# Optimization experiments

Measured on AMD Instinct MI355X. Metric: run time of the kernel, lower is better.

## Reference

```python
import math
import jax, jax.numpy as jnp
import numpy as np

B, S, E, H = 4, 2048, 1024, 16
D = E // H


def setup_inputs() -> dict:
    key = jax.random.key(0)
    k1, k2, k3 = jax.random.split(key, 3)
    return {
        "hidden_state": jax.random.normal(k1, (B, S, E), dtype=jnp.float32),
        "attention_mask": jnp.zeros((B, 1, 1, S), dtype=jnp.float32),
        "W_attn": jax.random.normal(k2, (E, 3 * E), dtype=jnp.float32) * 0.02,
        "b_attn": jnp.zeros((3 * E,), dtype=jnp.float32),
        "W_proj": jax.random.normal(k3, (E, E), dtype=jnp.float32) * 0.02,
        "b_proj": jnp.zeros((E,), dtype=jnp.float32),
    }


def reference(hidden_state, attention_mask, W_attn, b_attn, W_proj, b_proj):
    b, s, e = hidden_state.shape
    d = e // H
    # c_attn (HF Conv1D): x @ W + b -> [B,S,3E]
    x = hidden_state @ W_attn + b_attn
    q, k, v = jnp.split(x, 3, axis=-1)
    # split heads -> [B,H,S,D]
    q = q.reshape(b, s, H, d).transpose(0, 2, 1, 3)
    k = k.reshape(b, s, H, d).transpose(0, 2, 1, 3)
    v = v.reshape(b, s, H, d).transpose(0, 2, 1, 3)
    # scores [B,H,S,S]; scale=True divides by sqrt(d_head)
    w = jnp.einsum("bhqd,bhkd->bhqk", q, k) / math.sqrt(d)
    causal = jnp.tril(jnp.ones((s, s), dtype=w.dtype))[None, None]
    w = w * causal + (-10000.0) * (1.0 - causal)
    w = w + attention_mask
    w = jax.nn.softmax(w, axis=-1)  # attn_dropout p=0 (eval)
    out = jnp.einsum("bhqk,bhkd->bhqd", w, v)
    # merge heads -> [B,S,E]
    out = out.transpose(0, 2, 1, 3).reshape(b, s, e)
    # c_proj; resid_dropout p=0 (eval)
    return out @ W_proj + b_proj
```

## Files before the change

### kernel.cpp

```cpp
#include <hip/hip_runtime.h>
#include <hip/hip_bf16.h>

typedef __attribute__((ext_vector_type(4))) float f32x4;
typedef __attribute__((ext_vector_type(8))) short bf16x8;

#define B_SZ  4
#define S_LEN 2048
#define EMB   1024
#define NH    16
#define DH    64
#define E3    3072
#define QKLD  2048
#define LOG2E 1.4426950408889634f
#define SC2   (0.125f * LOG2E)
#define MSTAT 14.0f

__device__ __forceinline__ void gload_lds16(const void* g, void* l) {
  __builtin_amdgcn_global_load_lds((const __attribute__((address_space(1))) void*)g,
                                   (__attribute__((address_space(3))) void*)l, 16, 0, 0);
}

__global__ void cvt_bf16_kernel(const float* __restrict__ in,
                                __hip_bfloat16* __restrict__ out, int n) {
  const int i = (blockIdx.x * 256 + threadIdx.x) * 4;
  if (i >= n) return;
  const float4 v = *(const float4*)(in + i);
  __align__(8) __hip_bfloat16 o[4];
  o[0] = __float2bfloat16(v.x); o[1] = __float2bfloat16(v.y);
  o[2] = __float2bfloat16(v.z); o[3] = __float2bfloat16(v.w);
  *(uint2*)(out + i) = *(const uint2*)o;
}

__global__ __launch_bounds__(256)
void transpose_cvt(const float* __restrict__ in, __hip_bfloat16* __restrict__ out,
                   int R, int C) {
  __shared__ float tile[32][33];
  const int tx = threadIdx.x & 31, ty = threadIdx.x >> 5;
  const int c = blockIdx.x * 32 + tx;
#pragma unroll
  for (int i = 0; i < 32; i += 8)
    tile[ty + i][tx] = in[(size_t)(blockIdx.y * 32 + ty + i) * C + c];
  __syncthreads();
  const int r2 = blockIdx.y * 32 + tx;
#pragma unroll
  for (int i = 0; i < 32; i += 8)
    out[(size_t)(blockIdx.x * 32 + ty + i) * R + r2] = __float2bfloat16(tile[tx][ty + i]);
}

__global__ __launch_bounds__(256)
void gemm_bt_f32(const __hip_bfloat16* __restrict__ A, const __hip_bfloat16* __restrict__ BT,
                 const float* __restrict__ bias, float* __restrict__ Cout,
                 int M, int N, int K, int ldc) {
  __shared__ __align__(16) __hip_bfloat16 As[128 * 32];
  __shared__ __align__(16) __hip_bfloat16 Bs[128 * 32];
  const int tid = threadIdx.x;
  const int lane = tid & 63, w = tid >> 6;
  const int lr = lane & 15, lg = lane >> 4;
  const int wr = w >> 1, wc = w & 1;
  const int m0 = blockIdx.x * 128, n0 = blockIdx.y * 128;

  f32x4 acc[4][4] = {};

  for (int k0 = 0; k0 < K; k0 += 32) {
    __syncthreads();
#pragma unroll
    for (int rr = 0; rr < 2; ++rr) {
      const int base = rr * 4096 + w * 1024;
      const int idx = base + lane * 16;
      const int row = idx >> 6;
      const int col = (idx & 63) >> 1;
      gload_lds16(A + (size_t)(m0 + row) * K + k0 + col, (char*)As + base);
      gload_lds16(BT + (size_t)(n0 + row) * K + k0 + col, (char*)Bs + base);
    }
    __syncthreads();
    bf16x8 af[4], bg[4];
#pragma unroll
    for (int m = 0; m < 4; ++m)
      af[m] = *(const bf16x8*)&As[(wr * 64 + m * 16 + lr) * 32 + lg * 8];
#pragma unroll
    for (int n = 0; n < 4; ++n)
      bg[n] = *(const bf16x8*)&Bs[(wc * 64 + n * 16 + lr) * 32 + lg * 8];
#pragma unroll
    for (int m = 0; m < 4; ++m)
#pragma unroll
      for (int n = 0; n < 4; ++n)
        acc[m][n] = __builtin_amdgcn_mfma_f32_16x16x32_bf16(af[m], bg[n], acc[m][n], 0, 0, 0);
  }

#pragma unroll
  for (int m = 0; m < 4; ++m)
#pragma unroll
    for (int n = 0; n < 4; ++n) {
      const int col = n0 + wc * 64 + n * 16 + lr;
      const float bv = bias[col];
#pragma unroll
      for (int r = 0; r < 4; ++r) {
        const int rowg = m0 + wr * 64 + m * 16 + lg * 4 + r;
        Cout[(size_t)rowg * ldc + col] = acc[m][n][r] + bv;
      }
    }
}


#define SBAR() { __builtin_amdgcn_s_barrier(); __builtin_amdgcn_sched_barrier(0); }
#define VMCNT(N) asm volatile("s_waitcnt vmcnt(" #N ")" ::: "memory")

#define STG_A(T, H, BUF) { \
    const __hip_bfloat16* s_ = pA + (size_t)((H) * 128) * 1024 + (T) * 64; \
    gload_lds16(s_, (BUF) + (H) * 16384 + w * 1024 + lane * 16); \
    gload_lds16(s_ + 65536, (BUF) + (H) * 16384 + 8192 + w * 1024 + lane * 16); }

#define STG_B(T, H, BUF) { \
    const __hip_bfloat16* s_ = pB + (size_t)((H) * 128) * 1024 + (T) * 64; \
    gload_lds16(s_, (BUF) + (H) * 16384 + w * 1024 + lane * 16); \
    gload_lds16(s_ + 65536, (BUF) + (H) * 16384 + 8192 + w * 1024 + lane * 16); }

#define RD_A(BUF, MH) { _Pragma("unroll") for (int m_ = 0; m_ < 4; ++m_) { \
    a[m_][0] = *(const bf16x8*)((BUF) + arow + ((MH) * 64 + m_ * 16) * 128 + sw0); \
    a[m_][1] = *(const bf16x8*)((BUF) + arow + ((MH) * 64 + m_ * 16) * 128 + sw1); } }

#define RD_B(BUF, NH, BARR) { _Pragma("unroll") for (int n_ = 0; n_ < 2; ++n_) { \
    BARR[n_][0] = *(const bf16x8*)((BUF) + brow + ((NH) * 32 + n_ * 16) * 128 + sw0); \
    BARR[n_][1] = *(const bf16x8*)((BUF) + brow + ((NH) * 32 + n_ * 16) * 128 + sw1); } }

#define MQUAD(MH, NH, BARR) { __builtin_amdgcn_s_setprio(1); \
    _Pragma("unroll") for (int m_ = 0; m_ < 4; ++m_) \
    _Pragma("unroll") for (int n_ = 0; n_ < 2; ++n_) \
    _Pragma("unroll") for (int k_ = 0; k_ < 2; ++k_) \
      acc[(MH)*4+m_][(NH)*2+n_] = __builtin_amdgcn_mfma_f32_16x16x32_bf16( \
          a[m_][k_], BARR[n_][k_], acc[(MH)*4+m_][(NH)*2+n_], 0, 0, 0); \
    __builtin_amdgcn_s_setprio(0); }

__global__ __launch_bounds__(512, 2)
void gemm_qkv_8ph(const __hip_bfloat16* __restrict__ A, const __hip_bfloat16* __restrict__ BT,
                  const float* __restrict__ bias, __hip_bfloat16* __restrict__ qkOut,
                  __hip_bfloat16* __restrict__ vt) {
  __shared__ __attribute__((aligned(16))) char lds[131072];
  char* const As0 = lds;
  char* const As1 = lds + 32768;
  char* const Bs0 = lds + 65536;
  char* const Bs1 = lds + 98304;

  const int tid = threadIdx.x;
  const int lane = tid & 63, w = tid >> 6;
  const int lr = lane & 15, lg = lane >> 4, lg4 = lg * 4;
  const int wm = w >> 2, wn = w & 3;
  const int m0 = blockIdx.x * 256, n0 = blockIdx.y * 256;

  const int srl = lane >> 3;
  const int scol = ((lane & 7) ^ srl) * 8;
  const __hip_bfloat16* pA = A + (size_t)(m0 + w * 8 + srl) * 1024 + scol;
  const __hip_bfloat16* pB = BT + (size_t)(n0 + w * 8 + srl) * 1024 + scol;

  const int sw0 = (lg ^ (lr & 7)) << 4;
  const int sw1 = sw0 ^ 0x40;
  const int arow = (wm * 128 + lr) * 128;
  const int brow = (wn * 64 + lr) * 128;

  f32x4 acc[8][4] = {};
  bf16x8 a[4][2], b0[2][2], b1[2][2];

  STG_A(0, 0, As0); STG_B(0, 0, Bs0); STG_A(0, 1, As0); STG_B(0, 1, Bs0); STG_A(1, 0, As1);
  VMCNT(2);
  SBAR();

  auto iter = [&](int t0, bool more) {
    RD_A(As0, 0); RD_B(Bs0, 0, b0);
    STG_B(t0 + 1, 0, Bs1);
    SBAR(); MQUAD(0, 0, b0); SBAR();
    RD_B(Bs0, 1, b1);
    STG_A(t0 + 1, 1, As1);
    SBAR(); MQUAD(0, 1, b1); SBAR();
    RD_A(As0, 1); RD_B(Bs0, 0, b0);
    STG_B(t0 + 1, 1, Bs1);
    SBAR(); MQUAD(1, 0, b0); SBAR();
    RD_B(Bs0, 1, b1);
    if (more) { STG_A(t0 + 2, 0, As0); VMCNT(2); } else { VMCNT(0); }
    SBAR(); MQUAD(1, 1, b1); SBAR();
    RD_A(As1, 0); RD_B(Bs1, 0, b0);
    if (more) STG_B(t0 + 2, 0, Bs0);
    SBAR(); MQUAD(0, 0, b0); SBAR();
    RD_B(Bs1, 1, b1);
    if (more) STG_A(t0 + 2, 1, As0);
    SBAR(); MQUAD(0, 1, b1); SBAR();
    RD_A(As1, 1); RD_B(Bs1, 0, b0);
    if (more) STG_B(t0 + 2, 1, Bs0);
    SBAR(); MQUAD(1, 0, b0); SBAR();
    RD_B(Bs1, 1, b1);
    if (more) { STG_A(t0 + 3, 0, As1); VMCNT(2); }
    SBAR(); MQUAD(1, 1, b1); SBAR();
  };

#pragma unroll 1
  for (int i = 0; i < 7; ++i) iter(2 * i, true);
  iter(14, false);

  if (n0 >= 2 * EMB) {
#pragma unroll
    for (int m8 = 0; m8 < 8; ++m8) {
      const int rowg0 = m0 + wm * 128 + m8 * 16 + lg4;
      const int bz = rowg0 >> 11, sloc = rowg0 & (S_LEN - 1);
#pragma unroll
      for (int n4 = 0; n4 < 4; ++n4) {
        const int col = n0 + wn * 64 + n4 * 16 + lr;
        const int c2 = col - 2 * EMB;
        const int hh = c2 >> 6, dd = c2 & 63;
        const float bv = bias[col];
        __align__(8) __hip_bfloat16 pb[4];
#pragma unroll
        for (int r = 0; r < 4; ++r) pb[r] = __float2bfloat16(acc[m8][n4][r] + bv);
        *(uint2*)&vt[(size_t)((bz * NH + hh) * DH + dd) * S_LEN + sloc] = *(const uint2*)pb;
      }
    }
  } else {
#pragma unroll
    for (int m8 = 0; m8 < 8; ++m8) {
#pragma unroll
      for (int n4 = 0; n4 < 4; ++n4) {
        const int col = n0 + wn * 64 + n4 * 16 + lr;
        const float bv = bias[col];
#pragma unroll
        for (int r = 0; r < 4; ++r) {
          const int rowg = m0 + wm * 128 + m8 * 16 + lg4 + r;
          qkOut[(size_t)rowg * QKLD + col] = __float2bfloat16(acc[m8][n4][r] + bv);
        }
      }
    }
  }
}

template <bool DIAG>
__device__ __forceinline__ void qstep(const char* Ks, const char* Vs,
                                      __hip_bfloat16 (*Psw)[72], const float* Ms,
                                      int msoff, const bf16x8 (&aq)[2], f32x4 (&acc)[4],
                                      float& lrun, int lr, int lg, int lg4, int wq) {
  f32x4 sacc[4] = {};
  __builtin_amdgcn_s_setprio(1);
#pragma unroll
  for (int kt = 0; kt < 4; ++kt)
#pragma unroll
    for (int ks = 0; ks < 2; ++ks) {
      const bf16x8 kb = *(const bf16x8*)(Ks + (kt * 16 + lr) * 128 +
                                         (((ks * 4 + lg) ^ (lr & 7)) << 4));
      sacc[kt] = __builtin_amdgcn_mfma_f32_16x16x32_bf16(kb, aq[ks], sacc[kt], 0, 0, 0);
    }
  __builtin_amdgcn_s_setprio(0);
#pragma unroll
  for (int kt = 0; kt < 4; ++kt) {
    const f32x4 mk = *(const f32x4*)&Ms[msoff + kt * 16 + lg4];
    float pp[4];
    __align__(8) __hip_bfloat16 pb[4];
#pragma unroll
    for (int r = 0; r < 4; ++r) {
      float sv = sacc[kt][r] * SC2 + mk[r];
      if (DIAG && (kt * 16 + lg4 + r > wq)) sv = -1.0e9f;
      pp[r] = exp2f(sv);
      pb[r] = __float2bfloat16(pp[r]);
    }
    lrun += (pp[0] + pp[1]) + (pp[2] + pp[3]);
    *(uint2*)&Psw[lr][kt * 16 + lg4] = *(const uint2*)pb;
  }
#pragma unroll
  for (int ks = 0; ks < 2; ++ks) {
    const bf16x8 pa = *(const bf16x8*)&Psw[lr][ks * 32 + lg * 8];
    __builtin_amdgcn_s_setprio(1);
#pragma unroll
    for (int dt = 0; dt < 4; ++dt) {
      const bf16x8 vb = *(const bf16x8*)(Vs + (dt * 16 + lr) * 128 +
                                         (((ks * 4 + lg) ^ (lr & 7)) << 4));
      acc[dt] = __builtin_amdgcn_mfma_f32_16x16x32_bf16(pa, vb, acc[dt], 0, 0, 0);
    }
    __builtin_amdgcn_s_setprio(0);
  }
}

#define STAGE_LOAD_BUMP()                                                          \
  {                                                                                \
    kpre[0] = *(const bf16x8*)kcur;                                                \
    kpre[1] = *(const bf16x8*)(kcur + 8 * QKLD);                                   \
    vpre[0] = *(const bf16x8*)vcur;                                                \
    vpre[1] = *(const bf16x8*)(vcur + 8 * S_LEN);                                  \
    kcur += 64 * QKLD;                                                             \
    vcur += 64;                                                                    \
  }

#define TILE_SYNC(PREFETCH)                                                        \
  {                                                                                \
    __syncthreads();                                                               \
    *(bf16x8*)kw0 = kpre[0];                                                       \
    *(bf16x8*)(kw0 + 1024) = kpre[1];                                              \
    *(bf16x8*)vw0 = vpre[0];                                                       \
    *(bf16x8*)(vw0 + 1024) = vpre[1];                                              \
    __syncthreads();                                                               \
    if (PREFETCH) STAGE_LOAD_BUMP();                                               \
  }

__global__ __launch_bounds__(256, 4)
void flash_attn5(const __hip_bfloat16* __restrict__ qk, const __hip_bfloat16* __restrict__ vt,
                 const float* __restrict__ amask, __hip_bfloat16* __restrict__ aout) {
  const int x = blockIdx.x;
  const int h = blockIdx.y, bz = blockIdx.z;
  const int tid = threadIdx.x;
  const int lane = tid & 63, w = tid >> 6;
  const int lr = lane & 15, lg = lane >> 4, lg4 = lg * 4;
  const int wq = w * 16 + lr;

  const int qta = x, qtb = 31 - x;

  __shared__ __align__(16) __hip_bfloat16 Ks[64 * 64];
  __shared__ __align__(16) __hip_bfloat16 Vs[64 * 64];
  __shared__ __align__(16) __hip_bfloat16 Ps[4][16][72];
  __shared__ __align__(16) float Ms[S_LEN];

#pragma unroll
  for (int i = 0; i < 2; ++i) {
    const int e = (i * 256 + tid) * 4;
    const f32x4 mv = *(const f32x4*)&amask[bz * S_LEN + e];
    f32x4 r;
#pragma unroll
    for (int j = 0; j < 4; ++j) r[j] = mv[j] * LOG2E - MSTAT;
    *(f32x4*)&Ms[e] = r;
  }

  bf16x8 aqA[2], aqB[2];
  {
    const __hip_bfloat16* qpA =
        qk + (size_t)(bz * S_LEN + qta * 64 + w * 16 + lr) * QKLD + h * DH + lg * 8;
    aqA[0] = *(const bf16x8*)qpA; aqA[1] = *(const bf16x8*)(qpA + 32);
    const __hip_bfloat16* qpB =
        qk + (size_t)(bz * S_LEN + qtb * 64 + w * 16 + lr) * QKLD + h * DH + lg * 8;
    aqB[0] = *(const bf16x8*)qpB; aqB[1] = *(const bf16x8*)(qpB + 32);
  }

  f32x4 accA[4] = {}, accB[4] = {};
  float lA = 0.f, lB = 0.f;

  const __hip_bfloat16* kcur = qk + (size_t)bz * S_LEN * QKLD + EMB + h * DH +
                               (size_t)(w * 16 + (lane >> 3)) * QKLD + (lane & 7) * 8;
  const __hip_bfloat16* vcur = vt + (size_t)((bz * NH + h) * DH + w * 16 + (lane >> 3)) * S_LEN +
                               (lane & 7) * 8;
  char* kw0 = (char*)Ks + (w * 16 + (lane >> 3)) * 128 + (((lane & 7) ^ (lane >> 3)) << 4);
  char* vw0 = (char*)Vs + (w * 16 + (lane >> 3)) * 128 + (((lane & 7) ^ (lane >> 3)) << 4);

  bf16x8 kpre[2], vpre[2];
  STAGE_LOAD_BUMP();

  int msoff = 0;
  for (int t = 0; t < qta; ++t) {
    TILE_SYNC(true);
    qstep<false>((char*)Ks, (char*)Vs, Ps[w], Ms, msoff, aqA, accA, lA, lr, lg, lg4, wq);
    qstep<false>((char*)Ks, (char*)Vs, Ps[w], Ms, msoff, aqB, accB, lB, lr, lg, lg4, wq);
    msoff += 64;
  }
  TILE_SYNC(true);
  qstep<true>((char*)Ks, (char*)Vs, Ps[w], Ms, msoff, aqA, accA, lA, lr, lg, lg4, wq);
  qstep<false>((char*)Ks, (char*)Vs, Ps[w], Ms, msoff, aqB, accB, lB, lr, lg, lg4, wq);
  msoff += 64;
  for (int t = qta + 1; t < qtb; ++t) {
    TILE_SYNC(true);
    qstep<false>((char*)Ks, (char*)Vs, Ps[w], Ms, msoff, aqB, accB, lB, lr, lg, lg4, wq);
    msoff += 64;
  }
  TILE_SYNC(false);
  qstep<true>((char*)Ks, (char*)Vs, Ps[w], Ms, msoff, aqB, accB, lB, lr, lg, lg4, wq);

  lA += __shfl_xor(lA, 16); lA += __shfl_xor(lA, 32);
  lB += __shfl_xor(lB, 16); lB += __shfl_xor(lB, 32);
  float lqA[4], lqB[4];
#pragma unroll
  for (int r = 0; r < 4; ++r) {
    lqA[r] = __shfl(lA, lg4 + r);
    lqB[r] = __shfl(lB, lg4 + r);
  }
#pragma unroll
  for (int dt = 0; dt < 4; ++dt)
#pragma unroll
    for (int r = 0; r < 4; ++r) {
      const int qA = qta * 64 + w * 16 + lg4 + r;
      aout[(size_t)(bz * S_LEN + qA) * EMB + h * DH + dt * 16 + lr] =
          __float2bfloat16(accA[dt][r] / lqA[r]);
      const int qB = qtb * 64 + w * 16 + lg4 + r;
      aout[(size_t)(bz * S_LEN + qB) * EMB + h * DH + dt * 16 + lr] =
          __float2bfloat16(accB[dt][r] / lqB[r]);
    }
}

extern "C" void kernel_launch(void* const* d_in, const int* in_sizes, int n_in,
                              void* d_out, int out_size, void* d_ws, size_t ws_size,
                              hipStream_t stream) {
  const float* hidden = (const float*)d_in[0];
  const float* amask  = (const float*)d_in[1];
  const float* W_attn = (const float*)d_in[2];
  const float* b_attn = (const float*)d_in[3];
  const float* W_proj = (const float*)d_in[4];
  const float* b_proj = (const float*)d_in[5];
  float* out = (float*)d_out;

  char* ws = (char*)d_ws;
  __hip_bfloat16* hbf   = (__hip_bfloat16*)(ws);
  __hip_bfloat16* WaT   = (__hip_bfloat16*)(ws + 16777216);
  __hip_bfloat16* WpT   = (__hip_bfloat16*)(ws + 23068672);
  __hip_bfloat16* qkQK  = (__hip_bfloat16*)(ws + 25165824);
  __hip_bfloat16* vt    = (__hip_bfloat16*)(ws + 58720256);
  __hip_bfloat16* aoutb = (__hip_bfloat16*)(ws + 75497472);

  cvt_bf16_kernel<<<dim3(8192), dim3(256), 0, stream>>>(hidden, hbf, B_SZ * S_LEN * EMB);
  transpose_cvt<<<dim3(96, 32), dim3(256), 0, stream>>>(W_attn, WaT, EMB, E3);
  transpose_cvt<<<dim3(32, 32), dim3(256), 0, stream>>>(W_proj, WpT, EMB, EMB);
  gemm_qkv_8ph<<<dim3(32, 12), dim3(512), 0, stream>>>(hbf, WaT, b_attn, qkQK, vt);
  flash_attn5<<<dim3(16, NH, B_SZ), dim3(256), 0, stream>>>(qkQK, vt, amask, aoutb);
  gemm_bt_f32<<<dim3(64, 8), dim3(256), 0, stream>>>(aoutb, WpT, b_proj, out,
                                                     8192, EMB, EMB, EMB);
}
```

Measured before the change: 197.0 us.

## Interleave paired query tiles in one attention step and remap blocks for XCD locality

Adds qstep2, which computes scores, softmax and PV for both paired query tiles (A and B) in a single pass over the shared K/V tile. Each K/V fragment read from LDS then feeds two independent MFMA chains, and the two tiles get separate P buffers. The flash kernel also moves to a 1D grid whose index mapping groups blocks of the same head and batch onto the same XCD, aiming for better L2 reuse of K/V. The cost is more register pressure and extra LDS for the doubled P buffer.

```diff
diff --git a/kernel.cpp b/kernel.cpp
--- a/kernel.cpp
+++ b/kernel.cpp
@@ -100,7 +100,6 @@
       }
     }
 }
-
 
 #define SBAR() { __builtin_amdgcn_s_barrier(); __builtin_amdgcn_sched_barrier(0); }
 #define VMCNT(N) asm volatile("s_waitcnt vmcnt(" #N ")" ::: "memory")
@@ -229,6 +228,7 @@
   }
 }
 
+
 template <bool DIAG>
 __device__ __forceinline__ void qstep(const char* Ks, const char* Vs,
                                       __hip_bfloat16 (*Psw)[72], const float* Ms,
@@ -269,6 +269,59 @@
       const bf16x8 vb = *(const bf16x8*)(Vs + (dt * 16 + lr) * 128 +
                                          (((ks * 4 + lg) ^ (lr & 7)) << 4));
       acc[dt] = __builtin_amdgcn_mfma_f32_16x16x32_bf16(pa, vb, acc[dt], 0, 0, 0);
+    }
+    __builtin_amdgcn_s_setprio(0);
+  }
+}
+
+template <bool DIAGA>
+__device__ __forceinline__ void qstep2(const char* Ks, const char* Vs,
+                                       __hip_bfloat16 (*PsA)[72], __hip_bfloat16 (*PsB)[72],
+                                       const float* Ms, int msoff,
+                                       const bf16x8 (&aqA)[2], const bf16x8 (&aqB)[2],
+                                       f32x4 (&accA)[4], f32x4 (&accB)[4],
+                                       float& lA, float& lB, int lr, int lg, int lg4, int wq) {
+  f32x4 sA[4] = {}, sB[4] = {};
+  __builtin_amdgcn_s_setprio(1);
+#pragma unroll
+  for (int kt = 0; kt < 4; ++kt)
+#pragma unroll
+    for (int ks = 0; ks < 2; ++ks) {
+      const bf16x8 kb = *(const bf16x8*)(Ks + (kt * 16 + lr) * 128 +
+                                         (((ks * 4 + lg) ^ (lr & 7)) << 4));
+      sA[kt] = __builtin_amdgcn_mfma_f32_16x16x32_bf16(kb, aqA[ks], sA[kt], 0, 0, 0);
+      sB[kt] = __builtin_amdgcn_mfma_f32_16x16x32_bf16(kb, aqB[ks], sB[kt], 0, 0, 0);
+    }
+  __builtin_amdgcn_s_setprio(0);
+#pragma unroll
+  for (int kt = 0; kt < 4; ++kt) {
+    const f32x4 mk = *(const f32x4*)&Ms[msoff + kt * 16 + lg4];
+    float pA[4], pB[4];
+    __align__(8) __hip_bfloat16 bA[4], bB[4];
+#pragma unroll
+    for (int r = 0; r < 4; ++r) {
+      float svA = sA[kt][r] * SC2 + mk[r];
+      if (DIAGA && (kt * 16 + lg4 + r > wq)) svA = -1.0e9f;
+      const float svB = sB[kt][r] * SC2 + mk[r];
+      pA[r] = exp2f(svA); bA[r] = __float2bfloat16(pA[r]);
+      pB[r] = exp2f(svB); bB[r] = __float2bfloat16(pB[r]);
+    }
+    lA += (pA[0] + pA[1]) + (pA[2] + pA[3]);
+    lB += (pB[0] + pB[1]) + (pB[2] + pB[3]);
+    *(uint2*)&PsA[lr][kt * 16 + lg4] = *(const uint2*)bA;
+    *(uint2*)&PsB[lr][kt * 16 + lg4] = *(const uint2*)bB;
+  }
+#pragma unroll
+  for (int ks = 0; ks < 2; ++ks) {
+    const bf16x8 paA = *(const bf16x8*)&PsA[lr][ks * 32 + lg * 8];
+    const bf16x8 paB = *(const bf16x8*)&PsB[lr][ks * 32 + lg * 8];
+    __builtin_amdgcn_s_setprio(1);
+#pragma unroll
+    for (int dt = 0; dt < 4; ++dt) {
+      const bf16x8 vb = *(const bf16x8*)(Vs + (dt * 16 + lr) * 128 +
+                                         (((ks * 4 + lg) ^ (lr & 7)) << 4));
+      accA[dt] = __builtin_amdgcn_mfma_f32_16x16x32_bf16(paA, vb, accA[dt], 0, 0, 0);
+      accB[dt] = __builtin_amdgcn_mfma_f32_16x16x32_bf16(paB, vb, accB[dt], 0, 0, 0);
     }
     __builtin_amdgcn_s_setprio(0);
   }
@@ -296,10 +349,13 @@
   }
 
 __global__ __launch_bounds__(256, 4)
-void flash_attn5(const __hip_bfloat16* __restrict__ qk, const __hip_bfloat16* __restrict__ vt,
+void flash_attn6(const __hip_bfloat16* __restrict__ qk, const __hip_bfloat16* __restrict__ vt,
                  const float* __restrict__ amask, __hip_bfloat16* __restrict__ aout) {
-  const int x = blockIdx.x;
-  const int h = blockIdx.y, bz = blockIdx.z;
+  const int j = blockIdx.x;
+  const int g = (j & 7) + 8 * (j >> 7);
+  const int x = (j >> 3) & 15;
+  const int h = g >> 2, bz = g & 3;
+
   const int tid = threadIdx.x;
   const int lane = tid & 63, w = tid >> 6;
   const int lr = lane & 15, lg = lane >> 4, lg4 = lg * 4;
@@ -309,7 +365,7 @@
 
   __shared__ __align__(16) __hip_bfloat16 Ks[64 * 64];
   __shared__ __align__(16) __hip_bfloat16 Vs[64 * 64];
-  __shared__ __align__(16) __hip_bfloat16 Ps[4][16][72];
+  __shared__ __align__(16) __hip_bfloat16 Ps[4][2][16][72];
   __shared__ __align__(16) float Ms[S_LEN];
 
 #pragma unroll
@@ -318,7 +374,7 @@
     const f32x4 mv = *(const f32x4*)&amask[bz * S_LEN + e];
     f32x4 r;
 #pragma unroll
-    for (int j = 0; j < 4; ++j) r[j] = mv[j] * LOG2E - MSTAT;
+    for (int jj = 0; jj < 4; ++jj) r[jj] = mv[jj] * LOG2E - MSTAT;
     *(f32x4*)&Ms[e] = r;
   }
 
@@ -348,21 +404,21 @@
   int msoff = 0;
   for (int t = 0; t < qta; ++t) {
     TILE_SYNC(true);
-    qstep<false>((char*)Ks, (char*)Vs, Ps[w], Ms, msoff, aqA, accA, lA, lr, lg, lg4, wq);
-    qstep<false>((char*)Ks, (char*)Vs, Ps[w], Ms, msoff, aqB, accB, lB, lr, lg, lg4, wq);
+    qstep2<false>((char*)Ks, (char*)Vs, Ps[w][0], Ps[w][1], Ms, msoff,
+                  aqA, aqB, accA, accB, lA, lB, lr, lg, lg4, wq);
     msoff += 64;
   }
   TILE_SYNC(true);
-  qstep<true>((char*)Ks, (char*)Vs, Ps[w], Ms, msoff, aqA, accA, lA, lr, lg, lg4, wq);
-  qstep<false>((char*)Ks, (char*)Vs, Ps[w], Ms, msoff, aqB, accB, lB, lr, lg, lg4, wq);
+  qstep2<true>((char*)Ks, (char*)Vs, Ps[w][0], Ps[w][1], Ms, msoff,
+               aqA, aqB, accA, accB, lA, lB, lr, lg, lg4, wq);
   msoff += 64;
   for (int t = qta + 1; t < qtb; ++t) {
     TILE_SYNC(true);
-    qstep<false>((char*)Ks, (char*)Vs, Ps[w], Ms, msoff, aqB, accB, lB, lr, lg, lg4, wq);
+    qstep<false>((char*)Ks, (char*)Vs, Ps[w][1], Ms, msoff, aqB, accB, lB, lr, lg, lg4, wq);
     msoff += 64;
   }
   TILE_SYNC(false);
-  qstep<true>((char*)Ks, (char*)Vs, Ps[w], Ms, msoff, aqB, accB, lB, lr, lg, lg4, wq);
+  qstep<true>((char*)Ks, (char*)Vs, Ps[w][1], Ms, msoff, aqB, accB, lB, lr, lg, lg4, wq);
 
   lA += __shfl_xor(lA, 16); lA += __shfl_xor(lA, 32);
   lB += __shfl_xor(lB, 16); lB += __shfl_xor(lB, 32);
@@ -408,7 +464,7 @@
   transpose_cvt<<<dim3(96, 32), dim3(256), 0, stream>>>(W_attn, WaT, EMB, E3);
   transpose_cvt<<<dim3(32, 32), dim3(256), 0, stream>>>(W_proj, WpT, EMB, EMB);
   gemm_qkv_8ph<<<dim3(32, 12), dim3(512), 0, stream>>>(hbf, WaT, b_attn, qkQK, vt);
-  flash_attn5<<<dim3(16, NH, B_SZ), dim3(256), 0, stream>>>(qkQK, vt, amask, aoutb);
+  flash_attn6<<<dim3(1024), dim3(256), 0, stream>>>(qkQK, vt, amask, aoutb);
   gemm_bt_f32<<<dim3(64, 8), dim3(256), 0, stream>>>(aoutb, WpT, b_proj, out,
                                                      8192, EMB, EMB, EMB);
 }
```

Result: no change. 197.2 us (+0.1%).
